# Kernel optimization log

Hardware: AMD Instinct MI355X
Metric: run time of the kernel (lower is better)

Reference implementation:

```python
import jax, jax.numpy as jnp
import numpy as np

B = 4; N_LIG = 150; N_PROT = 550; N = 700
H = 128; HEADS = 4; KPH = 32; HPH = 32
L = 6; K = 48; EDGE_CH = 128; CUTOFF = 10.0
PROT_F = 27; NUM_CLASSES = 13
LOG2 = 0.6931471805599453
FLAT = N * H  # 89600, matches fc1 in_features


def ssp(x):
    # ShiftedSoftplus
    return jax.nn.softplus(x) - LOG2


def lin(x, w, b):
    # torch Linear convention: w is [out, in]
    return jnp.einsum('...i,oi->...o', x, w) + b


def setup_inputs() -> dict:
    key = jax.random.key(0)
    ki = iter(jax.random.split(key, 40))

    def nrm(shape, fan_in):
        return jax.random.normal(next(ki), shape, jnp.float32) / np.sqrt(fan_in).astype(np.float32)

    lig_pos = jax.random.normal(next(ki), (B, N_LIG, 3), jnp.float32) * 3.0
    lig_t = jax.random.randint(next(ki), (B, N_LIG, 1), 0, NUM_CLASSES).astype(jnp.float32)
    state = jnp.concatenate([lig_pos, lig_t], axis=-1)  # [B, N_LIG, 4]
    protein_pos_v = jnp.concatenate([
        jax.random.normal(next(ki), (B, N_PROT, 3), jnp.float32) * 3.0,
        jax.random.normal(next(ki), (B, N_PROT, PROT_F), jnp.float32)], axis=-1)  # [B, N_PROT, 30]

    inp = dict(state=state, protein_pos_v=protein_pos_v)
    inp['w_prot'] = nrm((H, PROT_F), PROT_F); inp['b_prot'] = jnp.zeros((H,), jnp.float32)
    inp['w_lig'] = nrm((H, NUM_CLASSES), NUM_CLASSES); inp['b_lig'] = jnp.zeros((H,), jnp.float32)
    # per-layer stacked encoder params (grouped 1x1 conv == per-head linear, no bias)
    inp['wq'] = nrm((L, HEADS, KPH, HPH), HPH)
    inp['wk'] = nrm((L, HEADS, KPH, HPH), HPH)
    inp['wv'] = nrm((L, HEADS, HPH, HPH), HPH)
    inp['wkn1_w'] = nrm((L, KPH, EDGE_CH), EDGE_CH); inp['wkn1_b'] = jnp.zeros((L, KPH), jnp.float32)
    inp['wkn2_w'] = nrm((L, KPH, KPH), KPH); inp['wkn2_b'] = jnp.zeros((L, KPH), jnp.float32)
    inp['wkl_w'] = nrm((L, KPH, KPH), KPH); inp['wkl_b'] = jnp.zeros((L, KPH), jnp.float32)
    inp['wvn1_w'] = nrm((L, HPH, EDGE_CH), EDGE_CH); inp['wvn1_b'] = jnp.zeros((L, HPH), jnp.float32)
    inp['wvn2_w'] = nrm((L, HPH, HPH), HPH); inp['wvn2_b'] = jnp.zeros((L, HPH), jnp.float32)
    inp['wvl_w'] = nrm((L, HPH, HPH), HPH); inp['wvl_b'] = jnp.zeros((L, HPH), jnp.float32)
    inp['cen_w'] = nrm((L, H, H), H); inp['cen_b'] = jnp.zeros((L, H), jnp.float32)
    inp['out_w'] = nrm((L, H, H), H); inp['out_b'] = jnp.zeros((L, H), jnp.float32)
    inp['ln_g'] = jnp.ones((L, H), jnp.float32); inp['ln_b'] = jnp.zeros((L, H), jnp.float32)
    inp['fc1_w'] = nrm((128, FLAT), FLAT); inp['fc1_b'] = jnp.zeros((128,), jnp.float32)
    inp['fc2_w'] = nrm((64, 128), 128); inp['fc2_b'] = jnp.zeros((64,), jnp.float32)
    inp['fc3_w'] = nrm((1, 64), 64); inp['fc3_b'] = jnp.zeros((1,), jnp.float32)
    return inp


def reference(state, protein_pos_v, w_prot, b_prot, w_lig, b_lig, wq, wk, wv,
              wkn1_w, wkn1_b, wkn2_w, wkn2_b, wkl_w, wkl_b,
              wvn1_w, wvn1_b, wvn2_w, wvn2_b, wvl_w, wvl_b,
              cen_w, cen_b, out_w, out_b, ln_g, ln_b,
              fc1_w, fc1_b, fc2_w, fc2_b, fc3_w, fc3_b):
    lig_pos = state[..., :3]
    lig_t = jax.lax.stop_gradient(state[..., 3]).astype(jnp.int32)
    lig_oh = jax.nn.one_hot(lig_t, NUM_CLASSES, dtype=jnp.float32)
    prot_pos = protein_pos_v[..., :3]
    prot_v = protein_pos_v[..., 3:]
    # compose_context: stable sort by batch -> protein atoms then ligand atoms per complex
    h = jnp.concatenate([lin(prot_v, w_prot, b_prot), lin(lig_oh, w_lig, b_lig)], axis=1)  # [B,N,H]
    pos = jnp.concatenate([prot_pos, lig_pos], axis=1)  # [B,N,3]
    # kNN graph (k nearest neighbors, no self loops), batched per complex
    d2 = jnp.sum((pos[:, :, None, :] - pos[:, None, :, :]) ** 2, axis=-1)  # [B,N,N]
    d2 = d2 + jnp.eye(N, dtype=d2.dtype) * 1e9
    _, nbr = jax.lax.top_k(-d2, K)  # [B,N,K]
    dist = jnp.sqrt(jnp.take_along_axis(d2, nbr, axis=2))  # [B,N,K]
    # Gaussian smearing of edge lengths
    offset = jnp.linspace(0.0, CUTOFF, EDGE_CH)
    coeff = -0.5 / (offset[1] - offset[0]) ** 2
    edge_attr = jnp.exp(coeff * (dist[..., None] - offset) ** 2)  # [B,N,K,E]
    gat = jax.vmap(lambda a, i: a[i])  # per-batch neighbor gather
    for l in range(L):
        xh = h.reshape(B, N, HEADS, HPH)
        q = jnp.einsum('bnhd,hkd->bnhk', xh, wq[l])
        kx = jnp.einsum('bnhd,hkd->bnhk', xh, wk[l])
        vx = jnp.einsum('bnhd,hkd->bnhk', xh, wv[l])
        w_k = lin(ssp(lin(edge_attr, wkn1_w[l], wkn1_b[l])), wkn2_w[l], wkn2_b[l])  # [B,N,K,KPH]
        keys_j = lin(w_k[:, :, :, None, :] * gat(kx, nbr), wkl_w[l], wkl_b[l])  # [B,N,K,heads,KPH]
        qk = jnp.einsum('bnhk,bnmhk->bnmh', q, keys_j)  # per-edge attention logits
        alpha = jax.nn.softmax(qk, axis=2)  # scatter_softmax over each node's K edges
        w_v = lin(ssp(lin(edge_attr, wvn1_w[l], wvn1_b[l])), wvn2_w[l], wvn2_b[l])  # [B,N,K,HPH]
        msg = lin(w_v[:, :, :, None, :] * gat(vx, nbr), wvl_w[l], wvl_b[l])  # [B,N,K,heads,HPH]
        aggr = jnp.einsum('bnmh,bnmhd->bnhd', alpha, msg).reshape(B, N, H)
        x = lin(h, cen_w[l], cen_b[l]) + aggr
        mu = jnp.mean(x, axis=-1, keepdims=True)
        var = jnp.var(x, axis=-1, keepdims=True)
        x = (x - mu) / jnp.sqrt(var + 1e-5) * ln_g[l] + ln_b[l]
        h = h + lin(ssp(x), out_w[l], out_b[l])  # residual per interaction block
    # decoup_batch + pad_tensor: constant 700 nodes/complex -> plain reshape
    x = h.reshape(B, FLAT)
    x = jax.nn.relu(lin(x, fc1_w, fc1_b))
    x = jax.nn.relu(lin(x, fc2_w, fc2_b))
    return lin(x, fc3_w, fc3_b)  # [B,1]
```

## Files before the change

kernel.cpp:

```cpp
#include <hip/hip_runtime.h>
#include <hip/hip_fp16.h>
#include <math.h>

constexpr int cB   = 4;
constexpr int cNL  = 150;
constexpr int cNP  = 550;
constexpr int cN   = 700;
constexpr int cH   = 128;
constexpr int cHeads = 4;
constexpr int cL   = 6;
constexpr int cK   = 48;
constexpr int cPF  = 27;
constexpr int cNC  = 13;
constexpr int cFLAT = cN * cH;
constexpr int cEdges = cB * cN * cK;

constexpr int   TABN = 4096;
#define TAB_DMAX 11.0f
#define TAB_HT   (TAB_DMAX / (float)(TABN - 1))
#define TAB_INV  ((float)(TABN - 1) / TAB_DMAX)

#define RBF_STEP (10.0f / 127.0f)
#define RBF_COEFF (-0.5f / (RBF_STEP * RBF_STEP))
#define LOG2F_C 0.69314718055994530942f

__device__ __forceinline__ float sspf(float x) {
    float ax = fabsf(x);
    return fmaxf(x, 0.0f) + __logf(1.0f + __expf(-ax)) - LOG2F_C;
}

__device__ __forceinline__ int mbcnt64(unsigned long long m) {
    return __builtin_amdgcn_mbcnt_hi((unsigned)(m >> 32),
           __builtin_amdgcn_mbcnt_lo((unsigned)m, 0));
}

__global__ void __launch_bounds__(256) k_init(
    const float* __restrict__ wq, const float* __restrict__ wk, const float* __restrict__ wv,
    const float* __restrict__ wkn1_w, const float* __restrict__ wvn1_w,
    const float* __restrict__ wkn2_w, const float* __restrict__ wvn2_w,
    const float* __restrict__ wvl_w,
    const float* __restrict__ cen_w, const float* __restrict__ out_w,
    float* __restrict__ wqT, float* __restrict__ wkT, float* __restrict__ wvT,
    float* __restrict__ w1Tk, float* __restrict__ w1Tv,
    float* __restrict__ w2Tk, float* __restrict__ w2Tv,
    float* __restrict__ wvlT,
    float* __restrict__ cenT, float* __restrict__ outT,
    const float* __restrict__ state, const float* __restrict__ ppv,
    const float* __restrict__ w_prot, const float* __restrict__ b_prot,
    const float* __restrict__ w_lig, const float* __restrict__ b_lig,
    float* __restrict__ h, float* __restrict__ pos)
{
    if (blockIdx.x < 1320) {
        int idx = blockIdx.x * 256 + threadIdx.x;
        if (idx < 3 * 24576) {
            int seg = idx / 24576, i = idx % 24576;
            const float* src = seg == 0 ? wq : (seg == 1 ? wk : wv);
            float* dst = seg == 0 ? wqT : (seg == 1 ? wkT : wvT);
            int l = i / 4096, r = i % 4096;
            int hh = r / 1024, r2 = r % 1024;
            int d = r2 / 32, k = r2 % 32;
            dst[i] = src[(((size_t)l * 4 + hh) * 32 + k) * 32 + d];
            return;
        }
        idx -= 3 * 24576;
        if (idx < 2 * 24576) {
            int seg = idx / 24576, i = idx % 24576;
            const float* src = seg == 0 ? wkn1_w : wvn1_w;
            float* dst = seg == 0 ? w1Tk : w1Tv;
            int l = i / 4096, r = i % 4096;
            int c = r / 32, o = r % 32;
            dst[i] = src[((size_t)l * 32 + o) * 128 + c];
            return;
        }
        idx -= 2 * 24576;
        if (idx < 3 * 6144) {
            int seg = idx / 6144, i = idx % 6144;
            const float* src = seg == 0 ? wkn2_w : (seg == 1 ? wvn2_w : wvl_w);
            float* dst = seg == 0 ? w2Tk : (seg == 1 ? w2Tv : wvlT);
            int l = i / 1024, r = i % 1024;
            int c = r / 32, o = r % 32;
            dst[i] = src[((size_t)l * 32 + o) * 32 + c];
            return;
        }
        idx -= 3 * 6144;
        int seg = idx / 98304, i = idx % 98304;
        const float* src = seg == 0 ? cen_w : out_w;
        float* dst = seg == 0 ? cenT : outT;
        int l = i / 16384, r = i % 16384;
        int ii = r / 128, o = r % 128;
        dst[i] = src[((size_t)l * 128 + o) * 128 + ii];
        return;
    }
    int rel = blockIdx.x - 1320;
    int node = rel * 2 + (threadIdx.x >> 7);
    int b = node / cN, n = node % cN;
    int o = threadIdx.x & 127;
    int lane = threadIdx.x & 63;
    float out;
    if (n < cNP) {
        const float* src = ppv + ((size_t)b * cNP + n) * 30;
        float v = (lane < 30) ? src[lane] : 0.f;
        float s = b_prot[o];
        #pragma unroll
        for (int f = 0; f < cPF; f++) s += w_prot[o * cPF + f] * __shfl(v, 3 + f);
        out = s;
        if (o < 3) pos[((size_t)b * cN + n) * 3 + o] = v;
    } else {
        int nl = n - cNP;
        const float* src = state + ((size_t)b * cNL + nl) * 4;
        float v = (lane < 4) ? src[lane] : 0.f;
        int t = (int)__shfl(v, 3);
        out = w_lig[o * cNC + t] + b_lig[o];
        if (o < 3) pos[((size_t)b * cN + n) * 3 + o] = v;
    }
    h[((size_t)b * cN + n) * cH + o] = out;
}

__global__ void __launch_bounds__(256) k_knn(
    const float* __restrict__ pos, int* __restrict__ nbr, float* __restrict__ dist,
    const float* __restrict__ w1Tk, const float* __restrict__ wkn1_b,
    const float* __restrict__ w2Tk, const float* __restrict__ wkn2_b,
    const float* __restrict__ w1Tv, const float* __restrict__ wvn1_b,
    const float* __restrict__ w2Tv, const float* __restrict__ wvn2_b,
    float* __restrict__ tab,
    const float* __restrict__ hbuf,
    const float* __restrict__ wqT, const float* __restrict__ wkT, const float* __restrict__ wvT,
    float* __restrict__ q0, __half* __restrict__ kx0, __half* __restrict__ vx0)
{
    int tid = threadIdx.x;
    if (blockIdx.x < cN) {
        int lane = tid & 63;
        int node = blockIdx.x * 4 + (tid >> 6);
        int b = node / cN, n = node % cN;
        const float* pb = pos + (size_t)b * cN * 3;
        float px = pb[n * 3 + 0], py = pb[n * 3 + 1], pz = pb[n * 3 + 2];
        float d2v[11];
        #pragma unroll
        for (int s = 0; s < 11; s++) {
            int j = lane + s * 64;
            float d2 = 1e30f;
            if (j < cN) {
                float dx = pb[j * 3 + 0] - px;
                float dy = pb[j * 3 + 1] - py;
                float dz = pb[j * 3 + 2] - pz;
                d2 = dx * dx + dy * dy + dz * dz;
                if (j == n) d2 = 1e9f;
            }
            d2v[s] = d2;
        }
        unsigned p = 0;
        for (int bit = 30; bit >= 0; --bit) {
            unsigned t = p | (1u << bit);
            int cnt = 0;
            #pragma unroll
            for (int s = 0; s < 11; s++)
                cnt += __popcll(__ballot(__float_as_uint(d2v[s]) < t));
            if (cnt <= 47) p = t;
        }
        int c_lt = 0;
        #pragma unroll
        for (int s = 0; s < 11; s++)
            c_lt += __popcll(__ballot(__float_as_uint(d2v[s]) < p));
        int base = 0, ebase = c_lt, need = 48 - c_lt;
        #pragma unroll
        for (int s = 0; s < 11; s++) {
            unsigned u = __float_as_uint(d2v[s]);
            unsigned long long blt = __ballot(u < p);
            unsigned long long beq = __ballot(u == p);
            int posn = -1;
            int bl = mbcnt64(blt);
            if (u < p) posn = base + bl;
            base += __popcll(blt);
            int r = mbcnt64(beq);
            int cs = __popcll(beq);
            int take = need < cs ? need : cs;
            if (u == p && r < take) posn = ebase + r;
            ebase += take; need -= take;
            if (posn >= 0) {
                nbr[(size_t)node * cK + posn] = s * 64 + lane;
                dist[(size_t)node * cK + posn] = sqrtf(d2v[s]);
            }
        }
        return;
    }
    if (blockIdx.x < cN + TABN / 4) {
        int rel = blockIdx.x - cN;
        int lane = tid & 63;
        int e = rel * 4 + (tid >> 6);
        int side = lane >> 5, o = lane & 31;
        float d = (float)e * TAB_HT;
        float z = d * (127.0f / 10.0f);
        int c0 = (int)floorf(z) - 7;
        c0 = c0 < 0 ? 0 : (c0 > 112 ? 112 : c0);
        int i = lane & 15;
        float tt = d - RBF_STEP * (float)(c0 + i);
        float eav = __expf(RBF_COEFF * tt * tt);
        const float* w1T = (side ? w1Tv : w1Tk);
        const float* b1  = (side ? wvn1_b : wkn1_b);
        const float* w2T = (side ? w2Tv : w2Tk);
        const float* b2  = (side ? wvn2_b : wkn2_b);
        int srcb = side * 32;
        for (int l = 0; l < cL; l++) {
            float s = b1[l * 32 + o];
            const float* w1p = w1T + (size_t)l * 4096;
            #pragma unroll
            for (int ii = 0; ii < 16; ii++)
                s += w1p[(c0 + ii) * 32 + o] * __shfl(eav, ii);
            float t1 = sspf(s);
            float s2 = b2[l * 32 + o];
            const float* w2p = w2T + (size_t)l * 1024;
            #pragma unroll
            for (int cc = 0; cc < 32; cc++)
                s2 += w2p[cc * 32 + o] * __shfl(t1, srcb + cc);
            tab[((size_t)(l * TABN + e) * 2 + side) * 32 + o] = s2;
        }
        return;
    }
    int bn = (blockIdx.x - cN - TABN / 4) * 2 + (tid >> 7);
    int o = tid & 127;
    int hh = o >> 5, kq = o & 31;
    float hval = hbuf[(size_t)bn * cH + o];
    size_t wo = ((size_t)0 * 4 + hh) * 1024;
    const float* bq = wqT + wo;
    const float* bk = wkT + wo;
    const float* bv = wvT + wo;
    int srcb = (hh & 1) * 32;
    float sq = 0.f, sk = 0.f, sv = 0.f;
    #pragma unroll
    for (int d = 0; d < 32; d++) {
        float x = __shfl(hval, srcb + d);
        sq += bq[d * 32 + kq] * x;
        sk += bk[d * 32 + kq] * x;
        sv += bv[d * 32 + kq] * x;
    }
    q0[(size_t)bn * cH + o] = sq;
    kx0[(size_t)bn * cH + o] = __float2half(sk);
    vx0[(size_t)bn * cH + o] = __float2half(sv);
}

__global__ void __launch_bounds__(256) k_attn(
    int l,
    const float* __restrict__ h_in, const float* __restrict__ qr,
    const __half* __restrict__ kxr, const __half* __restrict__ vxr,
    const int* __restrict__ nbr, const float* __restrict__ dist,
    const float* __restrict__ tab,
    const float* __restrict__ wkl_w,
    const float* __restrict__ wvlT, const float* __restrict__ wvl_b,
    const float* __restrict__ cenT, const float* __restrict__ cen_b,
    const float* __restrict__ outT, const float* __restrict__ out_b,
    const float* __restrict__ ln_g, const float* __restrict__ ln_b,
    float* __restrict__ h_out,
    float* __restrict__ qw, __half* __restrict__ kxw, __half* __restrict__ vxw,
    const float* __restrict__ wqT, const float* __restrict__ wkT, const float* __restrict__ wvT)
{
    int tid = threadIdx.x;
    int g = tid >> 7;
    int o = tid & 127;
    int bn = blockIdx.x * 2 + g;
    int b = bn / cN;
    int hh = o >> 5, c = o & 31;
    int srcb = (hh & 1) * 32;

    __shared__ float sh_h[2][cH];
    __shared__ float sh_qk[2][cK * cHeads];
    __shared__ float sh_t[2][cH];
    __shared__ int   sh_nb[2][cK];
    __shared__ int   sh_idx[2][cK];
    __shared__ float sh_frac[2][cK];
    __shared__ float red[2][4];

    sh_h[g][o] = h_in[(size_t)bn * cH + o];
    float qv = qr[(size_t)bn * cH + o];
    if (o < cK) {
        sh_nb[g][o] = nbr[(size_t)bn * cK + o];
        float d = dist[(size_t)bn * cK + o];
        float z = d * TAB_INV;
        int idx = (int)z;
        if (idx > TABN - 2) idx = TABN - 2;
        sh_idx[g][o] = idx;
        sh_frac[g][o] = fminf(z - (float)idx, 1.0f);
    }
    __syncthreads();

    const float* wklp = wkl_w + l * 1024;
    float qt = 0.f;
    #pragma unroll 8
    for (int k = 0; k < 32; k++) qt += __shfl(qv, srcb + k) * wklp[k * 32 + c];

    const __half* kxb = kxr + (size_t)b * cN * cH;
    const __half* vxb = vxr + (size_t)b * cN * cH;
    const float* tabl = tab + (size_t)l * TABN * 64;

    #pragma unroll 4
    for (int m = 0; m < cK; m += 2) {
        int j0 = sh_nb[g][m], j1 = sh_nb[g][m + 1];
        float k0 = __half2float(kxb[(size_t)j0 * cH + o]);
        float k1 = __half2float(kxb[(size_t)j1 * cH + o]);
        const float* t0 = tabl + (size_t)sh_idx[g][m] * 64 + c;
        const float* t1p = tabl + (size_t)sh_idx[g][m + 1] * 64 + c;
        float w0 = t0[0] + sh_frac[g][m] * (t0[64] - t0[0]);
        float w1 = t1p[0] + sh_frac[g][m + 1] * (t1p[64] - t1p[0]);
        float pa = qt * w0 * k0;
        float pb = qt * w1 * k1;
        float x = (c & 1) ? pb : pa;
        float y = (c & 1) ? pa : pb;
        x += __shfl_xor(y, 1);
        x += __shfl_xor(x, 2);
        x += __shfl_xor(x, 4);
        x += __shfl_xor(x, 8);
        x += __shfl_xor(x, 16);
        if (c < 2) sh_qk[g][(m + c) * cHeads + hh] = x;
    }
    __syncthreads();

    {
        float v1 = sh_qk[g][c * cHeads + hh];
        float v2 = (c < cK - 32) ? sh_qk[g][(32 + c) * cHeads + hh] : -1e30f;
        float mx = fmaxf(v1, v2);
        #pragma unroll
        for (int off = 16; off; off >>= 1) mx = fmaxf(mx, __shfl_xor(mx, off));
        float e1 = __expf(v1 - mx);
        float e2 = (c < cK - 32) ? __expf(v2 - mx) : 0.f;
        float s = e1 + e2;
        #pragma unroll
        for (int off = 16; off; off >>= 1) s += __shfl_xor(s, off);
        float inv = 1.0f / s;
        sh_qk[g][c * cHeads + hh] = e1 * inv;
        if (c < cK - 32) sh_qk[g][(32 + c) * cHeads + hh] = e2 * inv;
    }
    __syncthreads();

    float t = 0.f;
    #pragma unroll 4
    for (int m = 0; m < cK; m++) {
        int j = sh_nb[g][m];
        const float* tv = tabl + (size_t)sh_idx[g][m] * 64 + 32 + c;
        float wv_ = tv[0] + sh_frac[g][m] * (tv[64] - tv[0]);
        t += sh_qk[g][m * cHeads + hh] * (wv_ * __half2float(vxb[(size_t)j * cH + o]));
    }
    sh_t[g][o] = t;
    __syncthreads();

    const float* wvlTp = wvlT + l * 1024;
    float aggr = wvl_b[l * 32 + c];
    #pragma unroll 8
    for (int i = 0; i < 32; i++) aggr += wvlTp[i * 32 + c] * sh_t[g][hh * 32 + i];

    const float* cenTp = cenT + (size_t)l * cH * cH;
    float x0 = 0.f, x1 = 0.f;
    #pragma unroll 4
    for (int i = 0; i < cH; i += 2) {
        x0 += cenTp[i * cH + o] * sh_h[g][i];
        x1 += cenTp[(i + 1) * cH + o] * sh_h[g][i + 1];
    }
    float x = cen_b[l * cH + o] + aggr + x0 + x1;

    float s1 = x, s2 = x * x;
    #pragma unroll
    for (int off = 32; off; off >>= 1) {
        s1 += __shfl_xor(s1, off);
        s2 += __shfl_xor(s2, off);
    }
    int wid = (o >> 6);
    if ((o & 63) == 0) { red[g][wid * 2] = s1; red[g][wid * 2 + 1] = s2; }
    __syncthreads();
    float tot1 = red[g][0] + red[g][2], tot2 = red[g][1] + red[g][3];
    float mu = tot1 * (1.0f / 128.0f);
    float var = tot2 * (1.0f / 128.0f) - mu * mu;
    float xn = (x - mu) * rsqrtf(var + 1e-5f);
    xn = xn * ln_g[l * cH + o] + ln_b[l * cH + o];
    float sx = sspf(xn);
    sh_t[g][o] = sx;
    __syncthreads();

    const float* outTp = outT + (size_t)l * cH * cH;
    float o0 = 0.f, o1 = 0.f;
    #pragma unroll 4
    for (int i = 0; i < cH; i += 2) {
        o0 += outTp[i * cH + o] * sh_t[g][i];
        o1 += outTp[(i + 1) * cH + o] * sh_t[g][i + 1];
    }
    float hnew = sh_h[g][o] + out_b[l * cH + o] + o0 + o1;
    h_out[(size_t)bn * cH + o] = hnew;

    if (l < cL - 1) {
        size_t wo = ((size_t)(l + 1) * 4 + hh) * 1024;
        const float* bq = wqT + wo;
        const float* bk = wkT + wo;
        const float* bv = wvT + wo;
        float sq = 0.f, sk = 0.f, sv = 0.f;
        #pragma unroll
        for (int d = 0; d < 32; d++) {
            float xv = __shfl(hnew, srcb + d);
            sq += bq[d * 32 + c] * xv;
            sk += bk[d * 32 + c] * xv;
            sv += bv[d * 32 + c] * xv;
        }
        qw[(size_t)bn * cH + o] = sq;
        kxw[(size_t)bn * cH + o] = __float2half(sk);
        vxw[(size_t)bn * cH + o] = __float2half(sv);
    }
}

__global__ void __launch_bounds__(256) k_fc1p(const float* __restrict__ hbuf,
                                              const float* __restrict__ w,
                                              float* __restrict__ partial)
{
    int o = blockIdx.x >> 2, qp = blockIdx.x & 3;
    int tid = threadIdx.x;
    constexpr int CH = cFLAT / 4;
    const float4* wr = (const float4*)(w + (size_t)o * cFLAT + qp * CH);
    float a[4] = {0.f, 0.f, 0.f, 0.f};
    for (int i = tid; i < CH / 4; i += 256) {
        float4 wv = wr[i];
        #pragma unroll
        for (int bb = 0; bb < 4; bb++) {
            float4 hv = ((const float4*)(hbuf + (size_t)bb * cFLAT + qp * CH))[i];
            a[bb] += wv.x * hv.x + wv.y * hv.y + wv.z * hv.z + wv.w * hv.w;
        }
    }
    #pragma unroll
    for (int off = 32; off; off >>= 1) {
        #pragma unroll
        for (int bb = 0; bb < 4; bb++) a[bb] += __shfl_xor(a[bb], off);
    }
    __shared__ float red[4][4];
    if ((tid & 63) == 0) {
        #pragma unroll
        for (int bb = 0; bb < 4; bb++) red[tid >> 6][bb] = a[bb];
    }
    __syncthreads();
    if (tid < 4) {
        float s = red[0][tid] + red[1][tid] + red[2][tid] + red[3][tid];
        partial[((size_t)o * 4 + qp) * 4 + tid] = s;
    }
}

__global__ void __launch_bounds__(512) k_head2(const float* __restrict__ partial,
                                               const float* __restrict__ fc1_b,
                                               const float* __restrict__ fc2_w,
                                               const float* __restrict__ fc2_b,
                                               const float* __restrict__ fc3_w,
                                               const float* __restrict__ fc3_b,
                                               float* __restrict__ out)
{
    int tid = threadIdx.x;
    __shared__ float y1[4][128];
    __shared__ float y2[4][64];
    {
        int bb = tid >> 7, o = tid & 127;
        float s = fc1_b[o];
        #pragma unroll
        for (int qp = 0; qp < 4; qp++) s += partial[((size_t)o * 4 + qp) * 4 + bb];
        y1[bb][o] = fmaxf(s, 0.f);
    }
    __syncthreads();
    if (tid < 256) {
        int bb = tid >> 6, o = tid & 63;
        float s = fc2_b[o];
        #pragma unroll 8
        for (int i = 0; i < 128; i++) s += fc2_w[o * 128 + i] * y1[bb][i];
        y2[bb][o] = fmaxf(s, 0.f);
    }
    __syncthreads();
    if (tid < 4) {
        float s = fc3_b[0];
        #pragma unroll 8
        for (int i = 0; i < 64; i++) s += fc3_w[i] * y2[tid][i];
        out[tid] = s;
    }
}

extern "C" void kernel_launch(void* const* d_in, const int* in_sizes, int n_in,
                              void* d_out, int out_size, void* d_ws, size_t ws_size,
                              hipStream_t stream) {
    const float* state  = (const float*)d_in[0];
    const float* ppv    = (const float*)d_in[1];
    const float* w_prot = (const float*)d_in[2];
    const float* b_prot = (const float*)d_in[3];
    const float* w_lig  = (const float*)d_in[4];
    const float* b_lig  = (const float*)d_in[5];
    const float* wq     = (const float*)d_in[6];
    const float* wk     = (const float*)d_in[7];
    const float* wv     = (const float*)d_in[8];
    const float* wkn1_w = (const float*)d_in[9];
    const float* wkn1_b = (const float*)d_in[10];
    const float* wkn2_w = (const float*)d_in[11];
    const float* wkn2_b = (const float*)d_in[12];
    const float* wkl_w  = (const float*)d_in[13];
    const float* wvn1_w = (const float*)d_in[15];
    const float* wvn1_b = (const float*)d_in[16];
    const float* wvn2_w = (const float*)d_in[17];
    const float* wvn2_b = (const float*)d_in[18];
    const float* wvl_w  = (const float*)d_in[19];
    const float* wvl_b  = (const float*)d_in[20];
    const float* cen_w  = (const float*)d_in[21];
    const float* cen_b  = (const float*)d_in[22];
    const float* out_w  = (const float*)d_in[23];
    const float* out_b  = (const float*)d_in[24];
    const float* ln_g   = (const float*)d_in[25];
    const float* ln_b   = (const float*)d_in[26];
    const float* fc1_w  = (const float*)d_in[27];
    const float* fc1_b  = (const float*)d_in[28];
    const float* fc2_w  = (const float*)d_in[29];
    const float* fc2_b  = (const float*)d_in[30];
    const float* fc3_w  = (const float*)d_in[31];
    const float* fc3_b  = (const float*)d_in[32];

    float* ws = (float*)d_ws;
    size_t off = 0;
    float* pos   = ws + off; off += (size_t)cB * cN * 3;
    float* h_a   = ws + off; off += (size_t)cB * cN * cH;
    float* h_b   = ws + off; off += (size_t)cB * cN * cH;
    float* qA    = ws + off; off += (size_t)cB * cN * cH;
    float* qB    = ws + off; off += (size_t)cB * cN * cH;
    __half* kA   = (__half*)(ws + off); off += (size_t)cB * cN * cH / 2;
    __half* vA   = (__half*)(ws + off); off += (size_t)cB * cN * cH / 2;
    __half* kB   = (__half*)(ws + off); off += (size_t)cB * cN * cH / 2;
    __half* vB   = (__half*)(ws + off); off += (size_t)cB * cN * cH / 2;
    float* distb = ws + off; off += (size_t)cEdges;
    int*   nbrb  = (int*)(ws + off); off += (size_t)cEdges;
    float* tabb  = ws + off; off += (size_t)cL * TABN * 64;
    float* wqT   = ws + off; off += 24576;
    float* wkT   = ws + off; off += 24576;
    float* wvT   = ws + off; off += 24576;
    float* w1Tk  = ws + off; off += 24576;
    float* w1Tv  = ws + off; off += 24576;
    float* w2Tk  = ws + off; off += 6144;
    float* w2Tv  = ws + off; off += 6144;
    float* wvlT  = ws + off; off += 6144;
    float* cenT  = ws + off; off += 98304;
    float* outT  = ws + off; off += 98304;
    float* partial = ws + off; off += 2048;

    k_init<<<2720, 256, 0, stream>>>(wq, wk, wv, wkn1_w, wvn1_w, wkn2_w, wvn2_w,
                                     wvl_w, cen_w, out_w,
                                     wqT, wkT, wvT, w1Tk, w1Tv, w2Tk, w2Tv, wvlT, cenT, outT,
                                     state, ppv, w_prot, b_prot, w_lig, b_lig, h_a, pos);
    k_knn<<<cN + TABN / 4 + cB * cN / 2, 256, 0, stream>>>(
        pos, nbrb, distb,
        w1Tk, wkn1_b, w2Tk, wkn2_b, w1Tv, wvn1_b, w2Tv, wvn2_b, tabb,
        h_a, wqT, wkT, wvT, qA, kA, vA);

    float* hc = h_a;
    float* hn = h_b;
    for (int l = 0; l < cL; l++) {
        float* qr = (l & 1) ? qB : qA;
        __half* kr = (l & 1) ? kB : kA;
        __half* vr = (l & 1) ? vB : vA;
        float* qw2 = (l & 1) ? qA : qB;
        __half* kw2 = (l & 1) ? kA : kB;
        __half* vw2 = (l & 1) ? vA : vB;
        k_attn<<<cB * cN / 2, 256, 0, stream>>>(l, hc, qr, kr, vr, nbrb, distb, tabb,
            wkl_w, wvlT, wvl_b, cenT, cen_b, outT, out_b, ln_g, ln_b,
            hn, qw2, kw2, vw2, wqT, wkT, wvT);
        float* tmp = hc; hc = hn; hn = tmp;
    }

    k_fc1p<<<512, 256, 0, stream>>>(hc, fc1_w, partial);
    k_head2<<<1, 512, 0, stream>>>(partial, fc1_b, fc2_w, fc2_b, fc3_w, fc3_b, (float*)d_out);
}
```

Before: 308.1 us.

## Read weights row-major with float4, stage interpolated edge filters in LDS

Drops the pre-transpose of wq/wk/wv, cen, out and wvl weights in the init kernel. Each thread now reads its own weight row with float4 loads against LDS-resident activations, and wkl is transposed instead. The attention kernel also interpolates the per-edge key and value filter table entries once into a shared buffer, so the two edge loops no longer redo those global gathers. The costs are per-thread strided row reads, which are less coalesced than the old column reads, plus extra LDS and a barrier.

```diff
diff --git a/kernel.cpp b/kernel.cpp
--- a/kernel.cpp
+++ b/kernel.cpp
@@ -35,34 +35,19 @@
 }
 
 __global__ void __launch_bounds__(256) k_init(
-    const float* __restrict__ wq, const float* __restrict__ wk, const float* __restrict__ wv,
     const float* __restrict__ wkn1_w, const float* __restrict__ wvn1_w,
     const float* __restrict__ wkn2_w, const float* __restrict__ wvn2_w,
-    const float* __restrict__ wvl_w,
-    const float* __restrict__ cen_w, const float* __restrict__ out_w,
-    float* __restrict__ wqT, float* __restrict__ wkT, float* __restrict__ wvT,
+    const float* __restrict__ wkl_w,
     float* __restrict__ w1Tk, float* __restrict__ w1Tv,
     float* __restrict__ w2Tk, float* __restrict__ w2Tv,
-    float* __restrict__ wvlT,
-    float* __restrict__ cenT, float* __restrict__ outT,
+    float* __restrict__ wklT,
     const float* __restrict__ state, const float* __restrict__ ppv,
     const float* __restrict__ w_prot, const float* __restrict__ b_prot,
     const float* __restrict__ w_lig, const float* __restrict__ b_lig,
     float* __restrict__ h, float* __restrict__ pos)
 {
-    if (blockIdx.x < 1320) {
+    if (blockIdx.x < 264) {
         int idx = blockIdx.x * 256 + threadIdx.x;
-        if (idx < 3 * 24576) {
-            int seg = idx / 24576, i = idx % 24576;
-            const float* src = seg == 0 ? wq : (seg == 1 ? wk : wv);
-            float* dst = seg == 0 ? wqT : (seg == 1 ? wkT : wvT);
-            int l = i / 4096, r = i % 4096;
-            int hh = r / 1024, r2 = r % 1024;
-            int d = r2 / 32, k = r2 % 32;
-            dst[i] = src[(((size_t)l * 4 + hh) * 32 + k) * 32 + d];
-            return;
-        }
-        idx -= 3 * 24576;
         if (idx < 2 * 24576) {
             int seg = idx / 24576, i = idx % 24576;
             const float* src = seg == 0 ? wkn1_w : wvn1_w;
@@ -75,23 +60,15 @@
         idx -= 2 * 24576;
         if (idx < 3 * 6144) {
             int seg = idx / 6144, i = idx % 6144;
-            const float* src = seg == 0 ? wkn2_w : (seg == 1 ? wvn2_w : wvl_w);
-            float* dst = seg == 0 ? w2Tk : (seg == 1 ? w2Tv : wvlT);
+            const float* src = seg == 0 ? wkn2_w : (seg == 1 ? wvn2_w : wkl_w);
+            float* dst = seg == 0 ? w2Tk : (seg == 1 ? w2Tv : wklT);
             int l = i / 1024, r = i % 1024;
             int c = r / 32, o = r % 32;
             dst[i] = src[((size_t)l * 32 + o) * 32 + c];
-            return;
-        }
-        idx -= 3 * 6144;
-        int seg = idx / 98304, i = idx % 98304;
-        const float* src = seg == 0 ? cen_w : out_w;
-        float* dst = seg == 0 ? cenT : outT;
-        int l = i / 16384, r = i % 16384;
-        int ii = r / 128, o = r % 128;
-        dst[i] = src[((size_t)l * 128 + o) * 128 + ii];
+        }
         return;
     }
-    int rel = blockIdx.x - 1320;
+    int rel = blockIdx.x - 264;
     int node = rel * 2 + (threadIdx.x >> 7);
     int b = node / cN, n = node % cN;
     int o = threadIdx.x & 127;
@@ -124,7 +101,7 @@
     const float* __restrict__ w2Tv, const float* __restrict__ wvn2_b,
     float* __restrict__ tab,
     const float* __restrict__ hbuf,
-    const float* __restrict__ wqT, const float* __restrict__ wkT, const float* __restrict__ wvT,
+    const float* __restrict__ wq, const float* __restrict__ wk, const float* __restrict__ wv,
     float* __restrict__ q0, __half* __restrict__ kx0, __half* __restrict__ vx0)
 {
     int tid = threadIdx.x;
@@ -220,18 +197,22 @@
     int o = tid & 127;
     int hh = o >> 5, kq = o & 31;
     float hval = hbuf[(size_t)bn * cH + o];
-    size_t wo = ((size_t)0 * 4 + hh) * 1024;
-    const float* bq = wqT + wo;
-    const float* bk = wkT + wo;
-    const float* bv = wvT + wo;
+    size_t wo = ((size_t)hh * 32 + kq) * 32;
+    const float4* bq4 = (const float4*)(wq + wo);
+    const float4* bk4 = (const float4*)(wk + wo);
+    const float4* bv4 = (const float4*)(wv + wo);
     int srcb = (hh & 1) * 32;
     float sq = 0.f, sk = 0.f, sv = 0.f;
     #pragma unroll
-    for (int d = 0; d < 32; d++) {
-        float x = __shfl(hval, srcb + d);
-        sq += bq[d * 32 + kq] * x;
-        sk += bk[d * 32 + kq] * x;
-        sv += bv[d * 32 + kq] * x;
+    for (int i = 0; i < 8; i++) {
+        float4 a = bq4[i], b4 = bk4[i], v4 = bv4[i];
+        float x0 = __shfl(hval, srcb + 4 * i + 0);
+        float x1 = __shfl(hval, srcb + 4 * i + 1);
+        float x2 = __shfl(hval, srcb + 4 * i + 2);
+        float x3 = __shfl(hval, srcb + 4 * i + 3);
+        sq += a.x * x0 + a.y * x1 + a.z * x2 + a.w * x3;
+        sk += b4.x * x0 + b4.y * x1 + b4.z * x2 + b4.w * x3;
+        sv += v4.x * x0 + v4.y * x1 + v4.z * x2 + v4.w * x3;
     }
     q0[(size_t)bn * cH + o] = sq;
     kx0[(size_t)bn * cH + o] = __float2half(sk);
@@ -244,14 +225,14 @@
     const __half* __restrict__ kxr, const __half* __restrict__ vxr,
     const int* __restrict__ nbr, const float* __restrict__ dist,
     const float* __restrict__ tab,
-    const float* __restrict__ wkl_w,
-    const float* __restrict__ wvlT, const float* __restrict__ wvl_b,
-    const float* __restrict__ cenT, const float* __restrict__ cen_b,
-    const float* __restrict__ outT, const float* __restrict__ out_b,
+    const float* __restrict__ wklT,
+    const float* __restrict__ wvl_w, const float* __restrict__ wvl_b,
+    const float* __restrict__ cen_w, const float* __restrict__ cen_b,
+    const float* __restrict__ out_w, const float* __restrict__ out_b,
     const float* __restrict__ ln_g, const float* __restrict__ ln_b,
     float* __restrict__ h_out,
     float* __restrict__ qw, __half* __restrict__ kxw, __half* __restrict__ vxw,
-    const float* __restrict__ wqT, const float* __restrict__ wkT, const float* __restrict__ wvT)
+    const float* __restrict__ wq, const float* __restrict__ wk, const float* __restrict__ wv)
 {
     int tid = threadIdx.x;
     int g = tid >> 7;
@@ -261,13 +242,14 @@
     int hh = o >> 5, c = o & 31;
     int srcb = (hh & 1) * 32;
 
-    __shared__ float sh_h[2][cH];
+    __shared__ __align__(16) float sh_h[2][cH];
+    __shared__ __align__(16) float sh_t[2][cH];
     __shared__ float sh_qk[2][cK * cHeads];
-    __shared__ float sh_t[2][cH];
     __shared__ int   sh_nb[2][cK];
     __shared__ int   sh_idx[2][cK];
     __shared__ float sh_frac[2][cK];
     __shared__ float red[2][4];
+    __shared__ float w_s[2][cK][2][32];
 
     sh_h[g][o] = h_in[(size_t)bn * cH + o];
     float qv = qr[(size_t)bn * cH + o];
@@ -282,24 +264,42 @@
     }
     __syncthreads();
 
-    const float* wklp = wkl_w + l * 1024;
+    const float* tabl = tab + (size_t)l * TABN * 64;
+    #pragma unroll 4
+    for (int e = tid; e < 2 * cK * 64; e += 256) {
+        int c2 = e & 63;
+        int slot = e >> 6;
+        int gg = (slot >= cK) ? 1 : 0;
+        int m = slot - (gg ? cK : 0);
+        int idx = sh_idx[gg][m];
+        float f = sh_frac[gg][m];
+        const float* tp = tabl + (size_t)idx * 64 + c2;
+        float lo = tp[0], hi = tp[64];
+        ((float*)w_s)[e] = lo + f * (hi - lo);
+    }
+
+    const float4* wkl4 = (const float4*)(wklT + (size_t)l * 1024 + (size_t)c * 32);
     float qt = 0.f;
-    #pragma unroll 8
-    for (int k = 0; k < 32; k++) qt += __shfl(qv, srcb + k) * wklp[k * 32 + c];
+    #pragma unroll
+    for (int i = 0; i < 8; i++) {
+        float4 w4 = wkl4[i];
+        qt += w4.x * __shfl(qv, srcb + 4 * i + 0)
+            + w4.y * __shfl(qv, srcb + 4 * i + 1)
+            + w4.z * __shfl(qv, srcb + 4 * i + 2)
+            + w4.w * __shfl(qv, srcb + 4 * i + 3);
+    }
+    __syncthreads();
 
     const __half* kxb = kxr + (size_t)b * cN * cH;
     const __half* vxb = vxr + (size_t)b * cN * cH;
-    const float* tabl = tab + (size_t)l * TABN * 64;
-
-    #pragma unroll 4
+
+    #pragma unroll 8
     for (int m = 0; m < cK; m += 2) {
         int j0 = sh_nb[g][m], j1 = sh_nb[g][m + 1];
         float k0 = __half2float(kxb[(size_t)j0 * cH + o]);
         float k1 = __half2float(kxb[(size_t)j1 * cH + o]);
-        const float* t0 = tabl + (size_t)sh_idx[g][m] * 64 + c;
-        const float* t1p = tabl + (size_t)sh_idx[g][m + 1] * 64 + c;
-        float w0 = t0[0] + sh_frac[g][m] * (t0[64] - t0[0]);
-        float w1 = t1p[0] + sh_frac[g][m + 1] * (t1p[64] - t1p[0]);
+        float w0 = w_s[g][m][0][c];
+        float w1 = w_s[g][m + 1][0][c];
         float pa = qt * w0 * k0;
         float pb = qt * w1 * k1;
         float x = (c & 1) ? pb : pa;
@@ -330,30 +330,39 @@
     }
     __syncthreads();
 
-    float t = 0.f;
-    #pragma unroll 4
-    for (int m = 0; m < cK; m++) {
-        int j = sh_nb[g][m];
-        const float* tv = tabl + (size_t)sh_idx[g][m] * 64 + 32 + c;
-        float wv_ = tv[0] + sh_frac[g][m] * (tv[64] - tv[0]);
-        t += sh_qk[g][m * cHeads + hh] * (wv_ * __half2float(vxb[(size_t)j * cH + o]));
-    }
-    sh_t[g][o] = t;
-    __syncthreads();
-
-    const float* wvlTp = wvlT + l * 1024;
-    float aggr = wvl_b[l * 32 + c];
+    float t0 = 0.f, t1 = 0.f;
     #pragma unroll 8
-    for (int i = 0; i < 32; i++) aggr += wvlTp[i * 32 + c] * sh_t[g][hh * 32 + i];
-
-    const float* cenTp = cenT + (size_t)l * cH * cH;
-    float x0 = 0.f, x1 = 0.f;
-    #pragma unroll 4
-    for (int i = 0; i < cH; i += 2) {
-        x0 += cenTp[i * cH + o] * sh_h[g][i];
-        x1 += cenTp[(i + 1) * cH + o] * sh_h[g][i + 1];
-    }
-    float x = cen_b[l * cH + o] + aggr + x0 + x1;
+    for (int m = 0; m < cK; m += 2) {
+        int j0 = sh_nb[g][m], j1 = sh_nb[g][m + 1];
+        float v0 = __half2float(vxb[(size_t)j0 * cH + o]);
+        float v1 = __half2float(vxb[(size_t)j1 * cH + o]);
+        t0 += sh_qk[g][m * cHeads + hh] * (w_s[g][m][1][c] * v0);
+        t1 += sh_qk[g][(m + 1) * cHeads + hh] * (w_s[g][m + 1][1][c] * v1);
+    }
+    sh_t[g][o] = t0 + t1;
+    __syncthreads();
+
+    const float4* wvp4 = (const float4*)(wvl_w + (size_t)l * 1024 + (size_t)c * 32);
+    const float4* st4 = (const float4*)&sh_t[g][hh * 32];
+    float a0 = 0.f, a1 = 0.f, a2 = 0.f, a3 = 0.f;
+    #pragma unroll
+    for (int i = 0; i < 8; i++) {
+        float4 w4 = wvp4[i];
+        float4 t4 = st4[i];
+        a0 += w4.x * t4.x; a1 += w4.y * t4.y; a2 += w4.z * t4.z; a3 += w4.w * t4.w;
+    }
+    float aggr = wvl_b[l * 32 + c] + ((a0 + a1) + (a2 + a3));
+
+    const float4* cw4 = (const float4*)(cen_w + ((size_t)l * cH + o) * cH);
+    const float4* hh4 = (const float4*)sh_h[g];
+    float c0a = 0.f, c1a = 0.f, c2a = 0.f, c3a = 0.f;
+    #pragma unroll 8
+    for (int i = 0; i < 32; i++) {
+        float4 w4 = cw4[i];
+        float4 h4 = hh4[i];
+        c0a += w4.x * h4.x; c1a += w4.y * h4.y; c2a += w4.z * h4.z; c3a += w4.w * h4.w;
+    }
+    float x = cen_b[l * cH + o] + aggr + ((c0a + c1a) + (c2a + c3a));
 
     float s1 = x, s2 = x * x;
     #pragma unroll
@@ -373,28 +382,34 @@
     sh_t[g][o] = sx;
     __syncthreads();
 
-    const float* outTp = outT + (size_t)l * cH * cH;
-    float o0 = 0.f, o1 = 0.f;
-    #pragma unroll 4
-    for (int i = 0; i < cH; i += 2) {
-        o0 += outTp[i * cH + o] * sh_t[g][i];
-        o1 += outTp[(i + 1) * cH + o] * sh_t[g][i + 1];
-    }
-    float hnew = sh_h[g][o] + out_b[l * cH + o] + o0 + o1;
+    const float4* ow4 = (const float4*)(out_w + ((size_t)l * cH + o) * cH);
+    const float4* st4b = (const float4*)sh_t[g];
+    float o0 = 0.f, o1 = 0.f, o2 = 0.f, o3 = 0.f;
+    #pragma unroll 8
+    for (int i = 0; i < 32; i++) {
+        float4 w4 = ow4[i];
+        float4 t4 = st4b[i];
+        o0 += w4.x * t4.x; o1 += w4.y * t4.y; o2 += w4.z * t4.z; o3 += w4.w * t4.w;
+    }
+    float hnew = sh_h[g][o] + out_b[l * cH + o] + ((o0 + o1) + (o2 + o3));
     h_out[(size_t)bn * cH + o] = hnew;
 
     if (l < cL - 1) {
-        size_t wo = ((size_t)(l + 1) * 4 + hh) * 1024;
-        const float* bq = wqT + wo;
-        const float* bk = wkT + wo;
-        const float* bv = wvT + wo;
+        size_t wo = (((size_t)(l + 1) * 4 + hh) * 32 + c) * 32;
+        const float4* bq4 = (const float4*)(wq + wo);
+        const float4* bk4 = (const float4*)(wk + wo);
+        const float4* bv4 = (const float4*)(wv + wo);
         float sq = 0.f, sk = 0.f, sv = 0.f;
         #pragma unroll
-        for (int d = 0; d < 32; d++) {
-            float xv = __shfl(hnew, srcb + d);
-            sq += bq[d * 32 + c] * xv;
-            sk += bk[d * 32 + c] * xv;
-            sv += bv[d * 32 + c] * xv;
+        for (int i = 0; i < 8; i++) {
+            float4 a = bq4[i], b4 = bk4[i], v4 = bv4[i];
+            float x0 = __shfl(hnew, srcb + 4 * i + 0);
+            float x1 = __shfl(hnew, srcb + 4 * i + 1);
+            float x2 = __shfl(hnew, srcb + 4 * i + 2);
+            float x3 = __shfl(hnew, srcb + 4 * i + 3);
+            sq += a.x * x0 + a.y * x1 + a.z * x2 + a.w * x3;
+            sk += b4.x * x0 + b4.y * x1 + b4.z * x2 + b4.w * x3;
+            sv += v4.x * x0 + v4.y * x1 + v4.z * x2 + v4.w * x3;
         }
         qw[(size_t)bn * cH + o] = sq;
         kxw[(size_t)bn * cH + o] = __float2half(sk);
@@ -521,26 +536,21 @@
     float* distb = ws + off; off += (size_t)cEdges;
     int*   nbrb  = (int*)(ws + off); off += (size_t)cEdges;
     float* tabb  = ws + off; off += (size_t)cL * TABN * 64;
-    float* wqT   = ws + off; off += 24576;
-    float* wkT   = ws + off; off += 24576;
-    float* wvT   = ws + off; off += 24576;
     float* w1Tk  = ws + off; off += 24576;
     float* w1Tv  = ws + off; off += 24576;
     float* w2Tk  = ws + off; off += 6144;
     float* w2Tv  = ws + off; off += 6144;
-    float* wvlT  = ws + off; off += 6144;
-    float* cenT  = ws + off; off += 98304;
-    float* outT  = ws + off; off += 98304;
+    float* wklT  = ws + off; off += 6144;
     float* partial = ws + off; off += 2048;
 
-    k_init<<<2720, 256, 0, stream>>>(wq, wk, wv, wkn1_w, wvn1_w, wkn2_w, wvn2_w,
-                                     wvl_w, cen_w, out_w,
-                                     wqT, wkT, wvT, w1Tk, w1Tv, w2Tk, w2Tv, wvlT, cenT, outT,
-                                     state, ppv, w_prot, b_prot, w_lig, b_lig, h_a, pos);
+    k_init<<<264 + cB * cN / 2, 256, 0, stream>>>(
+        wkn1_w, wvn1_w, wkn2_w, wvn2_w, wkl_w,
+        w1Tk, w1Tv, w2Tk, w2Tv, wklT,
+        state, ppv, w_prot, b_prot, w_lig, b_lig, h_a, pos);
     k_knn<<<cN + TABN / 4 + cB * cN / 2, 256, 0, stream>>>(
         pos, nbrb, distb,
         w1Tk, wkn1_b, w2Tk, wkn2_b, w1Tv, wvn1_b, w2Tv, wvn2_b, tabb,
-        h_a, wqT, wkT, wvT, qA, kA, vA);
+        h_a, wq, wk, wv, qA, kA, vA);
 
     float* hc = h_a;
     float* hn = h_b;
@@ -552,8 +562,8 @@
         __half* kw2 = (l & 1) ? kA : kB;
         __half* vw2 = (l & 1) ? vA : vB;
         k_attn<<<cB * cN / 2, 256, 0, stream>>>(l, hc, qr, kr, vr, nbrb, distb, tabb,
-            wkl_w, wvlT, wvl_b, cenT, cen_b, outT, out_b, ln_g, ln_b,
-            hn, qw2, kw2, vw2, wqT, wkT, wvT);
+            wklT, wvl_w, wvl_b, cen_w, cen_b, out_w, out_b, ln_g, ln_b,
+            hn, qw2, kw2, vw2, wq, wk, wv);
         float* tmp = hc; hc = hn; hn = tmp;
     }
 
```

Result: slower. 640.5 us (+107.9%).

## Split each node across two thread groups in attention kernel

Applied to the files above, without the earlier changes.

The attention kernel previously processed two nodes per 256-thread block. Now each block handles one node, with the two 128-thread halves splitting the neighbor loop, the center and output matvecs, and the q/k/v projection, combining partial results through shared memory. This doubles the grid to 2800 blocks and halves the serial work per thread, aiming to cut latency per node on a kernel bound by gathers and dependent loads. The cost is extra syncthreads, shared-memory reductions and some redundant work such as the layernorm computed by both halves.

```diff
diff --git a/kernel.cpp b/kernel.cpp
--- a/kernel.cpp
+++ b/kernel.cpp
@@ -254,31 +254,33 @@
     const float* __restrict__ wqT, const float* __restrict__ wkT, const float* __restrict__ wvT)
 {
     int tid = threadIdx.x;
-    int g = tid >> 7;
+    int u = tid >> 7;
     int o = tid & 127;
-    int bn = blockIdx.x * 2 + g;
+    int bn = blockIdx.x;
     int b = bn / cN;
     int hh = o >> 5, c = o & 31;
     int srcb = (hh & 1) * 32;
 
-    __shared__ float sh_h[2][cH];
-    __shared__ float sh_qk[2][cK * cHeads];
-    __shared__ float sh_t[2][cH];
-    __shared__ int   sh_nb[2][cK];
-    __shared__ int   sh_idx[2][cK];
-    __shared__ float sh_frac[2][cK];
-    __shared__ float red[2][4];
-
-    sh_h[g][o] = h_in[(size_t)bn * cH + o];
+    __shared__ float sh_h[cH];
+    __shared__ float sh_t[cH];
+    __shared__ float sh_p[2][cH];
+    __shared__ float sh_c[2][cH];
+    __shared__ float sh_qk[cK * cHeads];
+    __shared__ int   sh_nb[cK];
+    __shared__ int   sh_idx[cK];
+    __shared__ float sh_frac[cK];
+    __shared__ float red[4][2];
+
     float qv = qr[(size_t)bn * cH + o];
-    if (o < cK) {
-        sh_nb[g][o] = nbr[(size_t)bn * cK + o];
+    if (u == 0) sh_h[o] = h_in[(size_t)bn * cH + o];
+    if (u == 1 && o < cK) {
+        sh_nb[o] = nbr[(size_t)bn * cK + o];
         float d = dist[(size_t)bn * cK + o];
         float z = d * TAB_INV;
         int idx = (int)z;
         if (idx > TABN - 2) idx = TABN - 2;
-        sh_idx[g][o] = idx;
-        sh_frac[g][o] = fminf(z - (float)idx, 1.0f);
+        sh_idx[o] = idx;
+        sh_frac[o] = fminf(z - (float)idx, 1.0f);
     }
     __syncthreads();
 
@@ -290,16 +292,18 @@
     const __half* kxb = kxr + (size_t)b * cN * cH;
     const __half* vxb = vxr + (size_t)b * cN * cH;
     const float* tabl = tab + (size_t)l * TABN * 64;
+    int mbase = u * (cK / 2);
 
     #pragma unroll 4
-    for (int m = 0; m < cK; m += 2) {
-        int j0 = sh_nb[g][m], j1 = sh_nb[g][m + 1];
+    for (int mi = 0; mi < cK / 2; mi += 2) {
+        int m = mbase + mi;
+        int j0 = sh_nb[m], j1 = sh_nb[m + 1];
         float k0 = __half2float(kxb[(size_t)j0 * cH + o]);
         float k1 = __half2float(kxb[(size_t)j1 * cH + o]);
-        const float* t0 = tabl + (size_t)sh_idx[g][m] * 64 + c;
-        const float* t1p = tabl + (size_t)sh_idx[g][m + 1] * 64 + c;
-        float w0 = t0[0] + sh_frac[g][m] * (t0[64] - t0[0]);
-        float w1 = t1p[0] + sh_frac[g][m + 1] * (t1p[64] - t1p[0]);
+        const float* t0 = tabl + (size_t)sh_idx[m] * 64 + c;
+        const float* t1p = tabl + (size_t)sh_idx[m + 1] * 64 + c;
+        float w0 = t0[0] + sh_frac[m] * (t0[64] - t0[0]);
+        float w1 = t1p[0] + sh_frac[m + 1] * (t1p[64] - t1p[0]);
         float pa = qt * w0 * k0;
         float pb = qt * w1 * k1;
         float x = (c & 1) ? pb : pa;
@@ -309,13 +313,13 @@
         x += __shfl_xor(x, 4);
         x += __shfl_xor(x, 8);
         x += __shfl_xor(x, 16);
-        if (c < 2) sh_qk[g][(m + c) * cHeads + hh] = x;
-    }
-    __syncthreads();
-
-    {
-        float v1 = sh_qk[g][c * cHeads + hh];
-        float v2 = (c < cK - 32) ? sh_qk[g][(32 + c) * cHeads + hh] : -1e30f;
+        if (c < 2) sh_qk[(m + c) * cHeads + hh] = x;
+    }
+    __syncthreads();
+
+    if (u == 0) {
+        float v1 = sh_qk[c * cHeads + hh];
+        float v2 = (c < cK - 32) ? sh_qk[(32 + c) * cHeads + hh] : -1e30f;
         float mx = fmaxf(v1, v2);
         #pragma unroll
         for (int off = 16; off; off >>= 1) mx = fmaxf(mx, __shfl_xor(mx, off));
@@ -325,35 +329,46 @@
         #pragma unroll
         for (int off = 16; off; off >>= 1) s += __shfl_xor(s, off);
         float inv = 1.0f / s;
-        sh_qk[g][c * cHeads + hh] = e1 * inv;
-        if (c < cK - 32) sh_qk[g][(32 + c) * cHeads + hh] = e2 * inv;
-    }
-    __syncthreads();
-
-    float t = 0.f;
+        sh_qk[c * cHeads + hh] = e1 * inv;
+        if (c < cK - 32) sh_qk[(32 + c) * cHeads + hh] = e2 * inv;
+    }
+    __syncthreads();
+
+    float t0a = 0.f, t1a = 0.f;
     #pragma unroll 4
-    for (int m = 0; m < cK; m++) {
-        int j = sh_nb[g][m];
-        const float* tv = tabl + (size_t)sh_idx[g][m] * 64 + 32 + c;
-        float wv_ = tv[0] + sh_frac[g][m] * (tv[64] - tv[0]);
-        t += sh_qk[g][m * cHeads + hh] * (wv_ * __half2float(vxb[(size_t)j * cH + o]));
-    }
-    sh_t[g][o] = t;
+    for (int mi = 0; mi < cK / 2; mi += 2) {
+        int m = mbase + mi;
+        int j0 = sh_nb[m], j1 = sh_nb[m + 1];
+        const float* tv0 = tabl + (size_t)sh_idx[m] * 64 + 32 + c;
+        const float* tv1 = tabl + (size_t)sh_idx[m + 1] * 64 + 32 + c;
+        float w0 = tv0[0] + sh_frac[m] * (tv0[64] - tv0[0]);
+        float w1 = tv1[0] + sh_frac[m + 1] * (tv1[64] - tv1[0]);
+        t0a += sh_qk[m * cHeads + hh] * (w0 * __half2float(vxb[(size_t)j0 * cH + o]));
+        t1a += sh_qk[(m + 1) * cHeads + hh] * (w1 * __half2float(vxb[(size_t)j1 * cH + o]));
+    }
+    sh_p[u][o] = t0a + t1a;
     __syncthreads();
 
     const float* wvlTp = wvlT + l * 1024;
-    float aggr = wvl_b[l * 32 + c];
-    #pragma unroll 8
-    for (int i = 0; i < 32; i++) aggr += wvlTp[i * 32 + c] * sh_t[g][hh * 32 + i];
+    float xpart = 0.f;
+    #pragma unroll
+    for (int i = u * 16; i < u * 16 + 16; i++)
+        xpart += wvlTp[i * 32 + c] * (sh_p[0][hh * 32 + i] + sh_p[1][hh * 32 + i]);
+    if (u == 0) xpart += wvl_b[l * 32 + c] + cen_b[l * cH + o];
 
     const float* cenTp = cenT + (size_t)l * cH * cH;
-    float x0 = 0.f, x1 = 0.f;
-    #pragma unroll 4
-    for (int i = 0; i < cH; i += 2) {
-        x0 += cenTp[i * cH + o] * sh_h[g][i];
-        x1 += cenTp[(i + 1) * cH + o] * sh_h[g][i + 1];
-    }
-    float x = cen_b[l * cH + o] + aggr + x0 + x1;
+    {
+        float x0 = 0.f, x1 = 0.f;
+        #pragma unroll 4
+        for (int i = u * 64; i < u * 64 + 64; i += 2) {
+            x0 += cenTp[i * cH + o] * sh_h[i];
+            x1 += cenTp[(i + 1) * cH + o] * sh_h[i + 1];
+        }
+        xpart += x0 + x1;
+    }
+    sh_c[u][o] = xpart;
+    __syncthreads();
+    float x = sh_c[0][o] + sh_c[1][o];
 
     float s1 = x, s2 = x * x;
     #pragma unroll
@@ -361,44 +376,53 @@
         s1 += __shfl_xor(s1, off);
         s2 += __shfl_xor(s2, off);
     }
-    int wid = (o >> 6);
-    if ((o & 63) == 0) { red[g][wid * 2] = s1; red[g][wid * 2 + 1] = s2; }
-    __syncthreads();
-    float tot1 = red[g][0] + red[g][2], tot2 = red[g][1] + red[g][3];
+    int wid = tid >> 6;
+    if ((tid & 63) == 0) { red[wid][0] = s1; red[wid][1] = s2; }
+    __syncthreads();
+    float tot1 = red[0][0] + red[1][0], tot2 = red[0][1] + red[1][1];
     float mu = tot1 * (1.0f / 128.0f);
     float var = tot2 * (1.0f / 128.0f) - mu * mu;
     float xn = (x - mu) * rsqrtf(var + 1e-5f);
     xn = xn * ln_g[l * cH + o] + ln_b[l * cH + o];
     float sx = sspf(xn);
-    sh_t[g][o] = sx;
+    if (u == 0) sh_t[o] = sx;
     __syncthreads();
 
     const float* outTp = outT + (size_t)l * cH * cH;
-    float o0 = 0.f, o1 = 0.f;
-    #pragma unroll 4
-    for (int i = 0; i < cH; i += 2) {
-        o0 += outTp[i * cH + o] * sh_t[g][i];
-        o1 += outTp[(i + 1) * cH + o] * sh_t[g][i + 1];
-    }
-    float hnew = sh_h[g][o] + out_b[l * cH + o] + o0 + o1;
-    h_out[(size_t)bn * cH + o] = hnew;
+    {
+        float o0 = 0.f, o1 = 0.f;
+        #pragma unroll 4
+        for (int i = u * 64; i < u * 64 + 64; i += 2) {
+            o0 += outTp[i * cH + o] * sh_t[i];
+            o1 += outTp[(i + 1) * cH + o] * sh_t[i + 1];
+        }
+        sh_c[u][o] = o0 + o1;
+    }
+    __syncthreads();
+    float hnew = sh_h[o] + out_b[l * cH + o] + sh_c[0][o] + sh_c[1][o];
+    if (u == 0) h_out[(size_t)bn * cH + o] = hnew;
 
     if (l < cL - 1) {
         size_t wo = ((size_t)(l + 1) * 4 + hh) * 1024;
-        const float* bq = wqT + wo;
-        const float* bk = wkT + wo;
-        const float* bv = wvT + wo;
-        float sq = 0.f, sk = 0.f, sv = 0.f;
-        #pragma unroll
-        for (int d = 0; d < 32; d++) {
-            float xv = __shfl(hnew, srcb + d);
-            sq += bq[d * 32 + c] * xv;
-            sk += bk[d * 32 + c] * xv;
-            sv += bv[d * 32 + c] * xv;
-        }
-        qw[(size_t)bn * cH + o] = sq;
-        kxw[(size_t)bn * cH + o] = __float2half(sk);
-        vxw[(size_t)bn * cH + o] = __float2half(sv);
+        if (u == 0) {
+            const float* bq = wqT + wo;
+            float sq = 0.f;
+            #pragma unroll
+            for (int d = 0; d < 32; d++) sq += bq[d * 32 + c] * __shfl(hnew, srcb + d);
+            qw[(size_t)bn * cH + o] = sq;
+        } else {
+            const float* bk = wkT + wo;
+            const float* bv = wvT + wo;
+            float sk = 0.f, sv = 0.f;
+            #pragma unroll
+            for (int d = 0; d < 32; d++) {
+                float xv = __shfl(hnew, srcb + d);
+                sk += bk[d * 32 + c] * xv;
+                sv += bv[d * 32 + c] * xv;
+            }
+            kxw[(size_t)bn * cH + o] = __float2half(sk);
+            vxw[(size_t)bn * cH + o] = __float2half(sv);
+        }
     }
 }
 
@@ -551,7 +575,7 @@
         float* qw2 = (l & 1) ? qA : qB;
         __half* kw2 = (l & 1) ? kA : kB;
         __half* vw2 = (l & 1) ? vA : vB;
-        k_attn<<<cB * cN / 2, 256, 0, stream>>>(l, hc, qr, kr, vr, nbrb, distb, tabb,
+        k_attn<<<cB * cN, 256, 0, stream>>>(l, hc, qr, kr, vr, nbrb, distb, tabb,
             wkl_w, wvlT, wvl_b, cenT, cen_b, outT, out_b, ln_g, ln_b,
             hn, qw2, kw2, vw2, wqT, wkT, wvT);
         float* tmp = hc; hc = hn; hn = tmp;
```

Result: slower. 324.0 us (+5.1%).

## Stage interpolated edge weights in LDS and split dense matvecs across node groups

Applied to the files above, without the earlier changes.

The interpolated edge-filter weights for both key and value paths are now computed once per block into shared memory by all 256 threads, instead of being re-read from the table in each attention loop. The cen/out/wvl matvecs are restructured so each 128-thread group handles half of the input dimension for both nodes in the block. Each weight row is then loaded once and used for two nodes, halving global weight traffic, and partial sums are combined through shared memory. This costs extra barriers and shared-memory space, which may lower occupancy.

```diff
diff --git a/kernel.cpp b/kernel.cpp
--- a/kernel.cpp
+++ b/kernel.cpp
@@ -261,13 +261,16 @@
     int hh = o >> 5, c = o & 31;
     int srcb = (hh & 1) * 32;
 
+    __shared__ float w_s[2][cK][2][32];
     __shared__ float sh_h[2][cH];
+    __shared__ float sh_t[2][cH];
     __shared__ float sh_qk[2][cK * cHeads];
-    __shared__ float sh_t[2][cH];
     __shared__ int   sh_nb[2][cK];
     __shared__ int   sh_idx[2][cK];
     __shared__ float sh_frac[2][cK];
     __shared__ float red[2][4];
+    float* w_flat = &w_s[0][0][0][0];
+    #define SH_C(gr, node, oo) w_flat[(((gr) << 1) | (node)) * cH + (oo)]
 
     sh_h[g][o] = h_in[(size_t)bn * cH + o];
     float qv = qr[(size_t)bn * cH + o];
@@ -287,19 +290,31 @@
     #pragma unroll 8
     for (int k = 0; k < 32; k++) qt += __shfl(qv, srcb + k) * wklp[k * 32 + c];
 
+    const float* tabl = tab + (size_t)l * TABN * 64;
+    #pragma unroll 4
+    for (int e = tid; e < 2 * cK * 64; e += 256) {
+        int c2 = e & 63;
+        int slot = e >> 6;
+        int gg = slot >= cK;
+        int m = slot - (gg ? cK : 0);
+        int idx = sh_idx[gg][m];
+        float f = sh_frac[gg][m];
+        const float* tp = tabl + (size_t)idx * 64 + c2;
+        float lo = tp[0], hi = tp[64];
+        w_flat[e] = lo + f * (hi - lo);
+    }
+    __syncthreads();
+
     const __half* kxb = kxr + (size_t)b * cN * cH;
     const __half* vxb = vxr + (size_t)b * cN * cH;
-    const float* tabl = tab + (size_t)l * TABN * 64;
 
     #pragma unroll 4
     for (int m = 0; m < cK; m += 2) {
         int j0 = sh_nb[g][m], j1 = sh_nb[g][m + 1];
         float k0 = __half2float(kxb[(size_t)j0 * cH + o]);
         float k1 = __half2float(kxb[(size_t)j1 * cH + o]);
-        const float* t0 = tabl + (size_t)sh_idx[g][m] * 64 + c;
-        const float* t1p = tabl + (size_t)sh_idx[g][m + 1] * 64 + c;
-        float w0 = t0[0] + sh_frac[g][m] * (t0[64] - t0[0]);
-        float w1 = t1p[0] + sh_frac[g][m + 1] * (t1p[64] - t1p[0]);
+        float w0 = w_s[g][m][0][c];
+        float w1 = w_s[g][m + 1][0][c];
         float pa = qt * w0 * k0;
         float pb = qt * w1 * k1;
         float x = (c & 1) ? pb : pa;
@@ -330,30 +345,37 @@
     }
     __syncthreads();
 
-    float t = 0.f;
+    float t0 = 0.f, t1 = 0.f;
     #pragma unroll 4
-    for (int m = 0; m < cK; m++) {
-        int j = sh_nb[g][m];
-        const float* tv = tabl + (size_t)sh_idx[g][m] * 64 + 32 + c;
-        float wv_ = tv[0] + sh_frac[g][m] * (tv[64] - tv[0]);
-        t += sh_qk[g][m * cHeads + hh] * (wv_ * __half2float(vxb[(size_t)j * cH + o]));
-    }
-    sh_t[g][o] = t;
+    for (int m = 0; m < cK; m += 2) {
+        int j0 = sh_nb[g][m], j1 = sh_nb[g][m + 1];
+        float v0 = __half2float(vxb[(size_t)j0 * cH + o]);
+        float v1 = __half2float(vxb[(size_t)j1 * cH + o]);
+        t0 += sh_qk[g][m * cHeads + hh] * (w_s[g][m][1][c] * v0);
+        t1 += sh_qk[g][(m + 1) * cHeads + hh] * (w_s[g][m + 1][1][c] * v1);
+    }
+    sh_t[g][o] = t0 + t1;
     __syncthreads();
 
     const float* wvlTp = wvlT + l * 1024;
-    float aggr = wvl_b[l * 32 + c];
-    #pragma unroll 8
-    for (int i = 0; i < 32; i++) aggr += wvlTp[i * 32 + c] * sh_t[g][hh * 32 + i];
-
+    float xp0 = 0.f, xp1 = 0.f;
+    #pragma unroll
+    for (int i = g * 16; i < g * 16 + 16; i++) {
+        float w = wvlTp[i * 32 + c];
+        xp0 += w * sh_t[0][hh * 32 + i];
+        xp1 += w * sh_t[1][hh * 32 + i];
+    }
     const float* cenTp = cenT + (size_t)l * cH * cH;
-    float x0 = 0.f, x1 = 0.f;
     #pragma unroll 4
-    for (int i = 0; i < cH; i += 2) {
-        x0 += cenTp[i * cH + o] * sh_h[g][i];
-        x1 += cenTp[(i + 1) * cH + o] * sh_h[g][i + 1];
-    }
-    float x = cen_b[l * cH + o] + aggr + x0 + x1;
+    for (int i = g * 64; i < g * 64 + 64; i++) {
+        float w = cenTp[i * cH + o];
+        xp0 += w * sh_h[0][i];
+        xp1 += w * sh_h[1][i];
+    }
+    SH_C(g, 0, o) = xp0;
+    SH_C(g, 1, o) = xp1;
+    __syncthreads();
+    float x = SH_C(0, g, o) + SH_C(1, g, o) + cen_b[l * cH + o] + wvl_b[l * 32 + c];
 
     float s1 = x, s2 = x * x;
     #pragma unroll
@@ -374,13 +396,17 @@
     __syncthreads();
 
     const float* outTp = outT + (size_t)l * cH * cH;
-    float o0 = 0.f, o1 = 0.f;
+    float op0 = 0.f, op1 = 0.f;
     #pragma unroll 4
-    for (int i = 0; i < cH; i += 2) {
-        o0 += outTp[i * cH + o] * sh_t[g][i];
-        o1 += outTp[(i + 1) * cH + o] * sh_t[g][i + 1];
-    }
-    float hnew = sh_h[g][o] + out_b[l * cH + o] + o0 + o1;
+    for (int i = g * 64; i < g * 64 + 64; i++) {
+        float w = outTp[i * cH + o];
+        op0 += w * sh_t[0][i];
+        op1 += w * sh_t[1][i];
+    }
+    SH_C(g, 0, o) = op0;
+    SH_C(g, 1, o) = op1;
+    __syncthreads();
+    float hnew = sh_h[g][o] + out_b[l * cH + o] + SH_C(0, g, o) + SH_C(1, g, o);
     h_out[(size_t)bn * cH + o] = hnew;
 
     if (l < cL - 1) {
@@ -400,6 +426,7 @@
         kxw[(size_t)bn * cH + o] = __float2half(sk);
         vxw[(size_t)bn * cH + o] = __float2half(sv);
     }
+    #undef SH_C
 }
 
 __global__ void __launch_bounds__(256) k_fc1p(const float* __restrict__ hbuf,
```

Result: slower. 386.4 us (+25.4%).
